# Kernel optimization log

Measured on AMD Instinct MI355X. Metric: run time of the kernel, lower is better.

Reference implementation:

```python
import jax, jax.numpy as jnp
import numpy as np
from jax import lax

# pywt db4 decomposition filters (hardcoded to avoid pywt dependency)
DB4_DEC_LO = np.array([-0.010597401784997278, 0.032883011666982945,
                       0.030841381835986965, -0.18703481171888114,
                       -0.02798376941698385, 0.6308807679295904,
                       0.7148465705525415, 0.23037781330885523], dtype=np.float32)
DB4_DEC_HI = np.array([-0.23037781330885523, 0.7148465705525415,
                       -0.6308807679295904, -0.02798376941698385,
                       0.18703481171888114, 0.030841381835986965,
                       -0.032883011666982945, -0.010597401784997278], dtype=np.float32)

B, T, C = 32, 16384, 64

def setup_inputs() -> dict:
    key = jax.random.key(0)
    x = jax.random.normal(key, (B, T, C), dtype=jnp.float32)
    return {"x": x,
            "dec_lo": jnp.asarray(DB4_DEC_LO),
            "dec_hi": jnp.asarray(DB4_DEC_HI)}

def _depthwise_conv1d(xp, filt, channels):
    # xp: [B, L, C]; filt: [K]; depthwise stride-2 valid cross-correlation
    k = jnp.broadcast_to(filt[:, None, None], (filt.shape[0], 1, channels))  # [K,1,C]
    return lax.conv_general_dilated(
        xp, k, window_strides=(2,), padding='VALID',
        dimension_numbers=('NWC', 'WIO', 'NWC'),
        feature_group_count=channels)

def reference(x, dec_lo, dec_hi):
    channels = x.shape[-1]
    filter_length = dec_lo.shape[0]          # 8 for db4
    pad = filter_length - 1                   # 7
    crop = pad // 2                           # 3
    xp = jnp.pad(x, ((0, 0), (pad, pad), (0, 0)), mode='reflect')
    approx = _depthwise_conv1d(xp, dec_lo, channels)[:, crop:-crop, :]
    detail = _depthwise_conv1d(xp, dec_hi, channels)[:, crop:-crop, :]
    # original concatenates all approx channels then all detail channels
    return jnp.concatenate([approx, detail], axis=-1)  # [B, T/2-2, 2C]
```

## Files before the change

### kernel.cpp

```cpp
#include <hip/hip_runtime.h>


#define BT    32
#define TT    16384
#define CC    64
#define T2    8190
#define OC    128
#define TB    64
#define NTILE ((T2 + TB - 1) / TB)
#define SLOTS 2304

typedef float vf4 __attribute__((ext_vector_type(4)));

__global__ __launch_bounds__(256, 4) void dwt_db4_lds_kernel(
    const float* __restrict__ x,
    const float* __restrict__ dec_lo,
    const float* __restrict__ dec_hi,
    float* __restrict__ out)
{
    __shared__ float lds[SLOTS * 4];

    const int tid  = threadIdx.x;
    const int tile = blockIdx.x;
    const int b    = blockIdx.y;

    const int t0 = tile * TB;
    const int m0 = 2 * t0 - 1;

    const float* __restrict__ xb = x + (size_t)b * TT * CC;

    float flo[8], fhi[8];
    #pragma unroll
    for (int k = 0; k < 8; ++k) { flo[k] = dec_lo[k]; fhi[k] = dec_hi[k]; }

    const int lane = tid & 63;
    const int wv   = tid >> 6;
    #pragma unroll
    for (int it = 0; it < 9; ++it) {
        const int base = it * 256 + wv * 64;
        const int slot = base + lane;
        const int r    = slot >> 4;
        const int c4   = (slot & 15) * 4;
        int m  = m0 + r;
        int mm = m < 0 ? -m : m;
        mm     = mm > (TT - 1) ? 2 * (TT - 1) - mm : mm;
        const float* gp = xb + (size_t)mm * CC + c4;
        __builtin_amdgcn_global_load_lds(
            (const __attribute__((address_space(1))) unsigned int*)gp,
            (__attribute__((address_space(3))) unsigned int*)&lds[(size_t)base * 4],
            16, 0, 0);
    }
    __syncthreads();

    const int cg = tid & 15;
    const int ts = tid >> 4;
    const int c4 = cg * 4;

    vf4 w[14];
    #pragma unroll
    for (int i = 0; i < 14; ++i)
        w[i] = *reinterpret_cast<const vf4*>(&lds[(size_t)(8 * ts + i) * CC + c4]);

    vf4 alo[4], ahi[4];
    #pragma unroll
    for (int j = 0; j < 4; ++j) { alo[j] = (vf4)0.0f; ahi[j] = (vf4)0.0f; }

    #pragma unroll
    for (int j = 0; j < 4; ++j) {
        #pragma unroll
        for (int k = 0; k < 8; ++k) {
            const vf4 v = w[2 * j + k];
            alo[j] += flo[k] * v;
            ahi[j] += fhi[k] * v;
        }
    }

    const int tbase = t0 + ts * 4;
    float* __restrict__ ob = out + (size_t)b * T2 * OC + (size_t)tbase * OC;
    #pragma unroll
    for (int j = 0; j < 4; ++j) {
        if (tbase + j < T2) {
            __builtin_nontemporal_store(alo[j],
                reinterpret_cast<vf4*>(ob + (size_t)j * OC + c4));
            __builtin_nontemporal_store(ahi[j],
                reinterpret_cast<vf4*>(ob + (size_t)j * OC + CC + c4));
        }
    }
}

extern "C" void kernel_launch(void* const* d_in, const int* in_sizes, int n_in,
                              void* d_out, int out_size, void* d_ws, size_t ws_size,
                              hipStream_t stream)
{
    const float* x      = (const float*)d_in[0];
    const float* dec_lo = (const float*)d_in[1];
    const float* dec_hi = (const float*)d_in[2];
    float*       out    = (float*)d_out;

    dim3 block(256);
    dim3 grid(NTILE, BT);

    hipLaunchKernelGGL(dwt_db4_lds_kernel, grid, block, 0, stream,
                       x, dec_lo, dec_hi, out);
}
```

Baseline: 231.9 us.

## Restructure DWT kernel into single-wave blocks with register-staged software pipeline

Replaces the 256-thread block that loaded one 64-output tile via global_load_lds with 64-thread single-wave blocks, each walking a strip of 8 consecutive 16-output steps. The next step's input rows are prefetched into registers while the current step computes and stores, then written to LDS. Because each block is one wave, no __syncthreads is needed. The aim is to overlap global loads with compute and stores. The trade-off is a large grid of small blocks, more per-thread register staging, and reliance on same-wave ordering of the LDS accesses.

```diff
diff --git a/kernel.cpp b/kernel.cpp
--- a/kernel.cpp
+++ b/kernel.cpp
@@ -6,84 +6,116 @@
 #define CC    64
 #define T2    8190
 #define OC    128
-#define TB    64
-#define NTILE ((T2 + TB - 1) / TB)
-#define SLOTS 2304
+#define WSTEP 16
+#define SROWS 40
+#define NLD   10
+#define STRIP 8
+#define NSTEP 512
+#define NW    (NSTEP / STRIP)
 
 typedef float vf4 __attribute__((ext_vector_type(4)));
 
-__global__ __launch_bounds__(256, 4) void dwt_db4_lds_kernel(
+__device__ __forceinline__ int reflect_row(int m) {
+    int mm = m < 0 ? -m : m;
+    return mm > (TT - 1) ? 2 * (TT - 1) - mm : mm;
+}
+
+__global__ __launch_bounds__(64) void dwt_db4_pipe_kernel(
     const float* __restrict__ x,
     const float* __restrict__ dec_lo,
     const float* __restrict__ dec_hi,
     float* __restrict__ out)
 {
-    __shared__ float lds[SLOTS * 4];
+    __shared__ float lds[SROWS * CC];
 
-    const int tid  = threadIdx.x;
-    const int tile = blockIdx.x;
+    const int lane = threadIdx.x;
+    const int w    = blockIdx.x;
     const int b    = blockIdx.y;
+    const int s0   = w * STRIP;
 
-    const int t0 = tile * TB;
-    const int m0 = 2 * t0 - 1;
-
-    const float* __restrict__ xb = x + (size_t)b * TT * CC;
+    const int cg = lane & 15;
+    const int ls = lane >> 4;
+    const int c4 = cg * 4;
 
     float flo[8], fhi[8];
     #pragma unroll
     for (int k = 0; k < 8; ++k) { flo[k] = dec_lo[k]; fhi[k] = dec_hi[k]; }
 
-    const int lane = tid & 63;
-    const int wv   = tid >> 6;
-    #pragma unroll
-    for (int it = 0; it < 9; ++it) {
-        const int base = it * 256 + wv * 64;
-        const int slot = base + lane;
-        const int r    = slot >> 4;
-        const int c4   = (slot & 15) * 4;
-        int m  = m0 + r;
-        int mm = m < 0 ? -m : m;
-        mm     = mm > (TT - 1) ? 2 * (TT - 1) - mm : mm;
-        const float* gp = xb + (size_t)mm * CC + c4;
-        __builtin_amdgcn_global_load_lds(
-            (const __attribute__((address_space(1))) unsigned int*)gp,
-            (__attribute__((address_space(3))) unsigned int*)&lds[(size_t)base * 4],
-            16, 0, 0);
-    }
-    __syncthreads();
+    const float* __restrict__ xb = x + (size_t)b * TT * CC;
 
-    const int cg = tid & 15;
-    const int ts = tid >> 4;
-    const int c4 = cg * 4;
+    const int sl_r = lane >> 4;
+    const int sl_c = (lane & 15) * 4;
 
-    vf4 w[14];
-    #pragma unroll
-    for (int i = 0; i < 14; ++i)
-        w[i] = *reinterpret_cast<const vf4*>(&lds[(size_t)(8 * ts + i) * CC + c4]);
+    vf4 stg[NLD];
 
-    vf4 alo[4], ahi[4];
-    #pragma unroll
-    for (int j = 0; j < 4; ++j) { alo[j] = (vf4)0.0f; ahi[j] = (vf4)0.0f; }
-
-    #pragma unroll
-    for (int j = 0; j < 4; ++j) {
+    {
+        const int mbase = 32 * s0 - 1;
         #pragma unroll
-        for (int k = 0; k < 8; ++k) {
-            const vf4 v = w[2 * j + k];
-            alo[j] += flo[k] * v;
-            ahi[j] += fhi[k] * v;
+        for (int it = 0; it < NLD; ++it) {
+            const int r  = it * 4 + sl_r;
+            const int mm = reflect_row(mbase + r);
+            stg[it] = *reinterpret_cast<const vf4*>(xb + (size_t)mm * CC + sl_c);
+        }
+        #pragma unroll
+        for (int it = 0; it < NLD; ++it) {
+            const int slot = it * 64 + lane;
+            *reinterpret_cast<vf4*>(&lds[slot * 4]) = stg[it];
         }
     }
 
-    const int tbase = t0 + ts * 4;
-    float* __restrict__ ob = out + (size_t)b * T2 * OC + (size_t)tbase * OC;
     #pragma unroll
-    for (int j = 0; j < 4; ++j) {
-        if (tbase + j < T2) {
-            __builtin_nontemporal_store(alo[j],
-                reinterpret_cast<vf4*>(ob + (size_t)j * OC + c4));
-            __builtin_nontemporal_store(ahi[j],
-                reinterpret_cast<vf4*>(ob + (size_t)j * OC + CC + c4));
+    for (int i = 0; i < STRIP; ++i) {
+        const int s = s0 + i;
+
+        if (i + 1 < STRIP) {
+            const int mbase = 32 * (s + 1) - 1;
+            #pragma unroll
+            for (int it = 0; it < NLD; ++it) {
+                const int r  = it * 4 + sl_r;
+                const int mm = reflect_row(mbase + r);
+                stg[it] = *reinterpret_cast<const vf4*>(xb + (size_t)mm * CC + sl_c);
+            }
+        }
+        __builtin_amdgcn_sched_barrier(0);
+
+        vf4 wnd[14];
+        #pragma unroll
+        for (int k = 0; k < 14; ++k)
+            wnd[k] = *reinterpret_cast<const vf4*>(&lds[(8 * ls + k) * CC + c4]);
+
+        vf4 alo[4], ahi[4];
+        #pragma unroll
+        for (int j = 0; j < 4; ++j) { alo[j] = (vf4)0.0f; ahi[j] = (vf4)0.0f; }
+
+        #pragma unroll
+        for (int j = 0; j < 4; ++j) {
+            #pragma unroll
+            for (int k = 0; k < 8; ++k) {
+                const vf4 v = wnd[2 * j + k];
+                alo[j] += flo[k] * v;
+                ahi[j] += fhi[k] * v;
+            }
+        }
+
+        const int tbase = WSTEP * s + 4 * ls;
+        float* __restrict__ ob = out + (size_t)b * T2 * OC + (size_t)tbase * OC;
+        #pragma unroll
+        for (int j = 0; j < 4; ++j) {
+            if (tbase + j < T2) {
+                __builtin_nontemporal_store(alo[j],
+                    reinterpret_cast<vf4*>(ob + (size_t)j * OC + c4));
+                __builtin_nontemporal_store(ahi[j],
+                    reinterpret_cast<vf4*>(ob + (size_t)j * OC + CC + c4));
+            }
+        }
+        __builtin_amdgcn_sched_barrier(0);
+
+        if (i + 1 < STRIP) {
+            #pragma unroll
+            for (int it = 0; it < NLD; ++it) {
+                const int slot = it * 64 + lane;
+                *reinterpret_cast<vf4*>(&lds[slot * 4]) = stg[it];
+            }
         }
     }
 }
@@ -97,9 +129,9 @@
     const float* dec_hi = (const float*)d_in[2];
     float*       out    = (float*)d_out;
 
-    dim3 block(256);
-    dim3 grid(NTILE, BT);
+    dim3 block(64);
+    dim3 grid(NW, BT);
 
-    hipLaunchKernelGGL(dwt_db4_lds_kernel, grid, block, 0, stream,
+    hipLaunchKernelGGL(dwt_db4_pipe_kernel, grid, block, 0, stream,
                        x, dec_lo, dec_hi, out);
 }
```

New measurement: 239.5 us. 1.03x slower.
